# Performance work log

Hardware: AMD Instinct MI355X
Metric: run time of the kernel (lower is better)

The kernel has to match this reference:

```python
import jax, jax.numpy as jnp
import numpy as np

S = 1            # support_num
NEIGHBOR = 32    # neighbor_num for ball query
EPS = 1e-12

def _gather(t, idx):
    # t: (bs, N, C), idx: (bs, M, n) -> (bs, M, n, C)
    return jax.vmap(lambda tb, ib: tb[ib])(t, idx)

def _pick(t, idx):
    # t: (bs, M, C), idx: (bs, V) -> (bs, V, C)
    return jax.vmap(lambda tb, ib: tb[ib])(t, idx)

def _normalize(x, axis):
    return x / jnp.maximum(jnp.linalg.norm(x, axis=axis, keepdims=True), EPS)

def query_ball_point(radius, nsample, xyz, new_xyz):
    # PointNet++-style ball query: indices of first nsample points within radius,
    # missing slots filled with the first valid neighbor (self, since dist=0).
    sq = jnp.sum((new_xyz[:, :, None, :] - xyz[:, None, :, :]) ** 2, axis=-1)  # (bs,S,N)
    N = xyz.shape[1]
    idx = jnp.broadcast_to(jnp.arange(N), sq.shape)
    idx = jnp.where(sq > radius * radius, N, idx)
    idx = jnp.sort(idx, axis=-1)[:, :, :nsample]
    return jnp.where(idx == N, idx[:, :, :1], idx)

def _dir_norm(vertices, nbr_idx):
    nbrs = _gather(vertices, nbr_idx)                       # (bs,v,n,3)
    return _normalize(nbrs - vertices[:, :, None, :], axis=-1)

def conv_surface(nbr_idx, vertices, directions, K=32):
    # directions: (3, S*K)
    dn = _dir_norm(vertices, nbr_idx)
    theta = jax.nn.relu(jnp.einsum('bvnd,dk->bvnk', dn, _normalize(directions, 0)))
    bs, v, n, _ = theta.shape
    return theta.reshape(bs, v, n, S, K).max(axis=2).sum(axis=2)  # (bs,v,K)

def conv_layer(nbr_idx, vertices, fm, w, b, d, K=32):
    # w: (Cin,(S+1)*K), b: ((S+1)*K,), d: (3,S*K)
    dn = _dir_norm(vertices, nbr_idx)
    theta = jax.nn.relu(jnp.einsum('bvnd,dk->bvnk', dn, _normalize(d, 0)))  # (bs,v,n,S*K)
    f = jnp.einsum('bvc,ck->bvk', fm, w) + b                # (bs,v,(S+1)*K)
    center, support = f[..., :K], f[..., K:]
    sup = _gather(support, nbr_idx)                          # (bs,v,n,S*K)
    bs, v, n, _ = sup.shape
    act = (theta * sup).reshape(bs, v, n, S, K).max(axis=2).sum(axis=2)
    return center + act

def pool_layer(vertices, fm, radius, key, rate=4, nn_num=4):
    idx = query_ball_point(radius, nn_num, vertices, vertices)
    pooled = _gather(fm, idx).max(axis=2)                    # neighborhood max-pool
    v = vertices.shape[1]
    perm = jax.random.permutation(key, v)[: v // rate]       # random subsample (fixed key)
    return vertices[:, perm], pooled[:, perm]

def get_nearest_index(target, source):
    sq = jnp.sum((target[:, :, None, :] - source[:, None, :, :]) ** 2, axis=-1)
    return jnp.argmin(sq, axis=-1)                           # (bs, V_target)

def _forward(vertices, onehot, d0, w1, b1, dd1, w2, b2, dd2, w3, b3, dd3,
             w4, b4, dd4, w5, b5, dd5, w6, b6, dd6, w7, b7, dd7,
             cw1, cb1, cw2, cb2, cw3, cb3):
    relu = jax.nn.relu
    bs, V, _ = vertices.shape
    ni = query_ball_point(0.25, NEIGHBOR, vertices, vertices)
    fm0 = relu(conv_surface(ni, vertices, d0))
    fm1 = jnp.concatenate([fm0, relu(conv_layer(ni, vertices, fm0, w1, b1, dd1))], -1)
    fm2 = jnp.concatenate([fm1, relu(conv_layer(ni, vertices, fm1, w2, b2, dd2))], -1)
    v1, fp1 = pool_layer(vertices, fm2, 0.25, jax.random.fold_in(jax.random.key(42), 1))
    ni = query_ball_point(0.39, NEIGHBOR, v1, v1)
    fm3 = jnp.concatenate([fp1, relu(conv_layer(ni, v1, fp1, w3, b3, dd3))], -1)
    fm4 = jnp.concatenate([fm3, relu(conv_layer(ni, v1, fm3, w4, b4, dd4))], -1)
    fm5 = jnp.concatenate([fm4, relu(conv_layer(ni, v1, fm4, w5, b5, dd5))], -1)
    v2, fp2 = pool_layer(v1, fm5, 0.39, jax.random.fold_in(jax.random.key(42), 2))
    ni = query_ball_point(0.63, NEIGHBOR, v2, v2)
    fm6 = jnp.concatenate([fp2, relu(conv_layer(ni, v2, fp2, w6, b6, dd6))], -1)
    fm7 = jnp.concatenate([fm6, relu(conv_layer(ni, v2, fm6, w7, b7, dd7))], -1)
    f_global = fm7.max(axis=1)                               # (bs, 256)
    n1 = get_nearest_index(vertices, v1)
    n2 = get_nearest_index(vertices, v2)
    fuse = jnp.concatenate([
        fm0, fm1, fm2,
        _pick(fm3, n1), _pick(fm4, n1), _pick(fm5, n1),
        _pick(fm6, n2), _pick(fm7, n2),
        jnp.broadcast_to(f_global[:, None, :], (bs, V, f_global.shape[-1])),
        jnp.broadcast_to(onehot[:, None, :], (bs, V, onehot.shape[-1])),
    ], axis=-1)                                              # (bs, V, 1424)
    h = relu(jnp.einsum('bvc,oc->bvo', fuse, cw1) + cb1)
    h = relu(jnp.einsum('bvc,oc->bvo', h, cw2) + cb2)
    return jnp.einsum('bvc,oc->bvo', h, cw3) + cb3           # (bs, V, class_num)


def setup_inputs() -> dict:
    key = jax.random.key(0)
    ks = iter(jax.random.split(key, 40))
    bs, N, cat = 8, 2048, 16
    vertices = jax.random.uniform(next(ks), (bs, N, 3), dtype=jnp.float32)
    labels = jax.random.randint(next(ks), (bs,), 0, cat)
    onehot = jax.nn.one_hot(labels, cat, dtype=jnp.float32)
    def p(shape):
        return jax.random.normal(next(ks), shape, dtype=jnp.float32) * 0.05
    inp = {"vertices": vertices, "onehot": onehot, "d0": p((3, S * 32))}
    ins = [32, 64, 96, 128, 160, 192, 224]
    for i, c in enumerate(ins, start=1):
        inp[f"w{i}"] = p((c, (S + 1) * 32))
        inp[f"b{i}"] = p(((S + 1) * 32,))
        inp[f"dd{i}"] = p((3, S * 32))
    inp["cw1"] = p((1024, 1424)); inp["cb1"] = p((1024,))
    inp["cw2"] = p((512, 1024)); inp["cb2"] = p((512,))
    inp["cw3"] = p((50, 512)); inp["cb3"] = p((50,))
    return inp


def reference(vertices, onehot, d0, w1, b1, dd1, w2, b2, dd2, w3, b3, dd3,
              w4, b4, dd4, w5, b5, dd5, w6, b6, dd6, w7, b7, dd7,
              cw1, cb1, cw2, cb2, cw3, cb3):
    return _forward(vertices, onehot, d0, w1, b1, dd1, w2, b2, dd2, w3, b3, dd3,
                    w4, b4, dd4, w5, b5, dd5, w6, b6, dd6, w7, b7, dd7,
                    cw1, cb1, cw2, cb2, cw3, cb3)
```

## Files before the change

### kernel.cpp

```cpp
#include <hip/hip_runtime.h>
#include <hip/hip_bf16.h>

#define BS 8
#define V0 2048
#define V1N 512
#define V2N 128

typedef unsigned short ushort_t;
typedef __attribute__((ext_vector_type(8))) short bf16x8;
typedef __attribute__((ext_vector_type(4))) float f32x4;

__device__ __forceinline__ void tf2x32(unsigned k0, unsigned k1,
                                       unsigned x0, unsigned x1,
                                       unsigned &o0, unsigned &o1) {
  unsigned ks2 = k0 ^ k1 ^ 0x1BD11BDAu;
  x0 += k0; x1 += k1;
#define RR(r) { x0 += x1; x1 = (x1 << (r)) | (x1 >> (32 - (r))); x1 ^= x0; }
  RR(13) RR(15) RR(26) RR(6)   x0 += k1;  x1 += ks2 + 1u;
  RR(17) RR(29) RR(16) RR(24)  x0 += ks2; x1 += k0 + 2u;
  RR(13) RR(15) RR(26) RR(6)   x0 += k0;  x1 += k1 + 3u;
  RR(17) RR(29) RR(16) RR(24)  x0 += k1;  x1 += ks2 + 4u;
  RR(13) RR(15) RR(26) RR(6)   x0 += ks2; x1 += k0 + 5u;
#undef RR
  o0 = x0; o1 = x1;
}

__device__ __forceinline__ ushort_t f2bf(float f) {
  unsigned u = __float_as_uint(f);
  u += 0x7FFFu + ((u >> 16) & 1u);
  return (ushort_t)(u >> 16);
}

__device__ __forceinline__ float sqdist_f32(float cx, float cy, float cz,
                                            const float* p) {
  float dx = __fsub_rn(cx, p[0]);
  float dy = __fsub_rn(cy, p[1]);
  float dz = __fsub_rn(cz, p[2]);
  return __fadd_rn(__fadd_rn(__fmul_rn(dx, dx), __fmul_rn(dy, dy)),
                   __fmul_rn(dz, dz));
}

#define KP1 1472

#define PREP_BLKS 1025
#define QBP1_BLKS 512
__global__ __launch_bounds__(256) void misc1_kernel(
    int* __restrict__ rank, const float* __restrict__ cw1,
    const float* __restrict__ cw2, const float* __restrict__ cw3,
    const float* __restrict__ cb3, ushort_t* __restrict__ cw1b,
    ushort_t* __restrict__ cw2b, ushort_t* __restrict__ cw3b,
    float* __restrict__ cb3p, const float* __restrict__ pts,
    int* __restrict__ ni1) {
  int bid = blockIdx.x, tid = threadIdx.x;
  if (bid < 18) {
    __shared__ unsigned sb[2048];
    int seg, segfirst, n, base;
    if (bid < 8)       { seg = 0; segfirst = 0;  n = 2048; base = 0; }
    else if (bid < 16) { seg = 1; segfirst = 8;  n = 2048; base = 2048; }
    else               { seg = 2; segfirst = 16; n = 512;  base = 4096; }
    unsigned k0, k1, nk0, nk1, sk0, sk1;
    if (seg == 0) {
      tf2x32(0u, 42u, 0u, 1u, k0, k1);
      tf2x32(k0, k1, 0u, 1u, sk0, sk1);
    } else if (seg == 1) {
      tf2x32(0u, 42u, 0u, 1u, k0, k1);
      tf2x32(k0, k1, 0u, 0u, nk0, nk1);
      tf2x32(nk0, nk1, 0u, 1u, sk0, sk1);
    } else {
      tf2x32(0u, 42u, 0u, 2u, k0, k1);
      tf2x32(k0, k1, 0u, 1u, sk0, sk1);
    }
    for (int i = tid; i < n; i += 256) {
      unsigned o0, o1;
      tf2x32(sk0, sk1, 0u, (unsigned)i, o0, o1);
      sb[i] = o0 ^ o1;
    }
    __syncthreads();
    int tt = (bid - segfirst) * 256 + tid;
    unsigned bt = sb[tt];
    int cnt = 0;
#pragma unroll 8
    for (int s = 0; s < n; ++s) {
      unsigned bs = sb[s];
      cnt += (bs < bt) || (bs == bt && s < tt);
    }
    rank[base + tt] = cnt;
  } else if (bid < 18 + PREP_BLKS) {
    int c = (bid - 18) * 256 + tid;
    const int C1 = 1024 * (KP1 / 8);
    const int C2 = (512 * 1024) / 8;
    const int C3 = (128 * 512) / 8;
    if (c < C1) {
      int n = c / (KP1 / 8);
      int cc = c - n * (KP1 / 8);
      int k = cc * 8;
      bf16x8 o = (bf16x8){0, 0, 0, 0, 0, 0, 0, 0};
      if (k < 1424) {
        const float* src = cw1 + (size_t)n * 1424 + k;
        float4 lo = *(const float4*)src;
        float4 hi = *(const float4*)(src + 4);
        o[0] = (short)f2bf(lo.x); o[1] = (short)f2bf(lo.y);
        o[2] = (short)f2bf(lo.z); o[3] = (short)f2bf(lo.w);
        o[4] = (short)f2bf(hi.x); o[5] = (short)f2bf(hi.y);
        o[6] = (short)f2bf(hi.z); o[7] = (short)f2bf(hi.w);
      }
      *(bf16x8*)(cw1b + (size_t)c * 8) = o;
    } else if (c < C1 + C2) {
      int u = (c - C1) * 8;
      const float* src = cw2 + u;
      float4 lo = *(const float4*)src;
      float4 hi = *(const float4*)(src + 4);
      bf16x8 o;
      o[0] = (short)f2bf(lo.x); o[1] = (short)f2bf(lo.y);
      o[2] = (short)f2bf(lo.z); o[3] = (short)f2bf(lo.w);
      o[4] = (short)f2bf(hi.x); o[5] = (short)f2bf(hi.y);
      o[6] = (short)f2bf(hi.z); o[7] = (short)f2bf(hi.w);
      *(bf16x8*)(cw2b + u) = o;
    } else if (c < C1 + C2 + C3) {
      int u = (c - C1 - C2) * 8;
      int n = u >> 9, k = u & 511;
      bf16x8 o = (bf16x8){0, 0, 0, 0, 0, 0, 0, 0};
      if (n < 50) {
        const float* src = cw3 + (size_t)n * 512 + k;
        float4 lo = *(const float4*)src;
        float4 hi = *(const float4*)(src + 4);
        o[0] = (short)f2bf(lo.x); o[1] = (short)f2bf(lo.y);
        o[2] = (short)f2bf(lo.z); o[3] = (short)f2bf(lo.w);
        o[4] = (short)f2bf(hi.x); o[5] = (short)f2bf(hi.y);
        o[6] = (short)f2bf(hi.z); o[7] = (short)f2bf(hi.w);
      }
      *(bf16x8*)(cw3b + u) = o;
    } else if (c < C1 + C2 + C3 + 16) {
      int u = (c - C1 - C2 - C3) * 8;
#pragma unroll
      for (int e = 0; e < 8; ++e)
        cb3p[u + e] = (u + e) < 50 ? cb3[u + e] : 0.f;
    }
  } else {
    __shared__ float spts[V0 * 3];
    int bq = bid - 18 - PREP_BLKS;
    int qbase = bq * 32;
    int b = qbase >> 11;
    const float* base = pts + (size_t)b * V0 * 3;
    for (int i = tid; i < V0 * 3 / 4; i += 256)
      ((float4*)spts)[i] = ((const float4*)base)[i];
    __syncthreads();
    int lane = tid & 63, wv = tid >> 6;
    for (int rep = 0; rep < 8; ++rep) {
      int qoff = wv * 8 + rep;
      int qi = (qbase & 2047) + qoff;
      int wid = qbase + qoff;
      float cx = spts[qi * 3], cy = spts[qi * 3 + 1], cz = spts[qi * 3 + 2];
      int cnt = 0, idx0 = 0;
      for (int j0 = 0; j0 < V0; j0 += 64) {
        int j = j0 + lane;
        float d2 = sqdist_f32(cx, cy, cz, spts + (size_t)j * 3);
        bool in = (d2 <= 0.0625f);
        unsigned long long mask = __ballot(in);
        if (cnt == 0 && mask) idx0 = j0 + __builtin_ctzll(mask);
        if (in) {
          int rk = cnt + __popcll(mask & ((1ull << lane) - 1ull));
          if (rk < 32) ni1[(size_t)wid * 32 + rk] = j;
        }
        cnt += __popcll(mask);
        if (cnt >= 32) break;
      }
      for (int s = cnt + lane; s < 32; s += 64) ni1[(size_t)wid * 32 + s] = idx0;
    }
  }
}

__device__ __forceinline__ void dirn(const float* base, int v, int nb,
                                     float& ox, float& oy, float& oz) {
  float dx = __fsub_rn(base[nb * 3 + 0], base[v * 3 + 0]);
  float dy = __fsub_rn(base[nb * 3 + 1], base[v * 3 + 1]);
  float dz = __fsub_rn(base[nb * 3 + 2], base[v * 3 + 2]);
  float s2 = __fadd_rn(__fadd_rn(__fmul_rn(dx, dx), __fmul_rn(dy, dy)),
                       __fmul_rn(dz, dz));
  float nrm = fmaxf(__fsqrt_rn(s2), 1e-12f);
  ox = __fdiv_rn(dx, nrm); oy = __fdiv_rn(dy, nrm); oz = __fdiv_rn(dz, nrm);
}

__device__ __forceinline__ void norm_col(const float* d, int k,
                                         float& ox, float& oy, float& oz) {
  float x = d[k], y = d[32 + k], z = d[64 + k];
  float s2 = __fadd_rn(__fadd_rn(__fmul_rn(x, x), __fmul_rn(y, y)),
                       __fmul_rn(z, z));
  float nrm = fmaxf(__fsqrt_rn(s2), 1e-12f);
  ox = __fdiv_rn(x, nrm); oy = __fdiv_rn(y, nrm); oz = __fdiv_rn(z, nrm);
}

__global__ __launch_bounds__(256) void misc2_kernel(
    const int* __restrict__ rank, int* __restrict__ perm1,
    int* __restrict__ perm2, const float* __restrict__ pts,
    const int* __restrict__ ni, const float* __restrict__ d0,
    const float* __restrict__ w1, const float* __restrict__ b1,
    float* __restrict__ out, float* __restrict__ fn) {
  int bid = blockIdx.x, tid = threadIdx.x;
  if (bid == 0) {
    __shared__ int a1[2048];
    __shared__ int a2[2048];
    for (int i = tid; i < 2048; i += 256) a1[rank[i]] = i;
    __syncthreads();
    for (int i = tid; i < 2048; i += 256) a2[rank[2048 + i]] = a1[i];
    __syncthreads();
    for (int i = tid; i < 512; i += 256) perm1[i] = a2[i];
    for (int i = tid; i < 512; i += 256) a1[rank[4096 + i]] = i;
    __syncthreads();
    for (int i = tid; i < 128; i += 256) perm2[i] = a1[i];
    return;
  }
  __shared__ float sdir[3][32];
  __shared__ float sdn[8][32][3];
  __shared__ float sfm[8][32];
  if (tid < 32) {
    float x, y, z; norm_col(d0, tid, x, y, z);
    sdir[0][tid] = x; sdir[1][tid] = y; sdir[2][tid] = z;
  }
  int vloc = tid >> 5, k = tid & 31;
  size_t bvg = (size_t)(bid - 1) * 8 + vloc;
  int b = (int)(bvg >> 11), v = (int)(bvg & 2047);
  const float* base = pts + (size_t)b * V0 * 3;
  int nb = ni[bvg * 32 + k];
  float x, y, z; dirn(base, v, nb, x, y, z);
  sdn[vloc][k][0] = x; sdn[vloc][k][1] = y; sdn[vloc][k][2] = z;
  __syncthreads();
  float m = 0.f;
  for (int n = 0; n < 32; ++n) {
    float d = sdn[vloc][n][0] * sdir[0][k] + sdn[vloc][n][1] * sdir[1][k] +
              sdn[vloc][n][2] * sdir[2][k];
    m = fmaxf(m, fmaxf(d, 0.f));
  }
  out[bvg * 96 + k] = m;
  sfm[vloc][k] = m;
  __syncthreads();
  float a1v = b1[k], a2v = b1[k + 32];
  for (int c = 0; c < 32; ++c) {
    float vv = sfm[vloc][c];
    a1v += vv * w1[c * 64 + k];
    a2v += vv * w1[c * 64 + k + 32];
  }
  fn[bvg * 64 + k] = a1v;
  fn[bvg * 64 + k + 32] = a2v;
}

__global__ __launch_bounds__(256) void conv_act_kernel(
    const float* __restrict__ pts, const float* __restrict__ dd,
    const int* __restrict__ ni, const float* __restrict__ f,
    float* __restrict__ out, int Nv, int ldout, int colofs,
    const float* __restrict__ wn, const float* __restrict__ bn,
    float* __restrict__ fn) {
  __shared__ float sdir[3][32];
  __shared__ float sdn[8][32][3];
  __shared__ int sidx[8][32];
  __shared__ float sfm[8][256];
  int tid = threadIdx.x;
  if (tid < 32) {
    float x, y, z; norm_col(dd, tid, x, y, z);
    sdir[0][tid] = x; sdir[1][tid] = y; sdir[2][tid] = z;
  }
  int vloc = tid >> 5, k = tid & 31;
  size_t bvg = (size_t)blockIdx.x * 8 + vloc;
  int b = (int)(bvg / Nv), v = (int)(bvg % Nv);
  const float* base = pts + (size_t)b * Nv * 3;
  int nb = ni[bvg * 32 + k];
  float x, y, z; dirn(base, v, nb, x, y, z);
  sdn[vloc][k][0] = x; sdn[vloc][k][1] = y; sdn[vloc][k][2] = z;
  sidx[vloc][k] = nb;
  __syncthreads();
  float m = -INFINITY;
  size_t fb = (size_t)b * Nv * 64;
  for (int n = 0; n < 32; ++n) {
    float th = fmaxf(sdn[vloc][n][0] * sdir[0][k] + sdn[vloc][n][1] * sdir[1][k] +
                     sdn[vloc][n][2] * sdir[2][k], 0.f);
    float sup = f[fb + (size_t)sidx[vloc][n] * 64 + 32 + k];
    m = fmaxf(m, th * sup);
  }
  float center = f[bvg * 64 + k];
  float res = fmaxf(center + m, 0.f);
  out[bvg * ldout + colofs + k] = res;
  if (wn) {
    size_t rowbase = (size_t)blockIdx.x * 8;
#pragma unroll 1
    for (int r = 0; r < 8; ++r)
      if (tid < colofs) sfm[r][tid] = out[(rowbase + r) * ldout + tid];
    sfm[vloc][colofs + k] = res;
    __syncthreads();
    int cin = colofs + 32;
    float a1v = bn[k], a2v = bn[k + 32];
    for (int c = 0; c < cin; ++c) {
      float vv = sfm[vloc][c];
      a1v += vv * wn[c * 64 + k];
      a2v += vv * wn[c * 64 + k + 32];
    }
    fn[bvg * 64 + k] = a1v;
    fn[bvg * 64 + k + 32] = a2v;
  }
}

__global__ __launch_bounds__(256) void conv_act_qbp_kernel(
    const float* __restrict__ pts, int Nv, float rrq,
    const float* __restrict__ dd, int* __restrict__ ni_out,
    const float* __restrict__ f, float* __restrict__ out, int ldout,
    int colofs, const float* __restrict__ wn, const float* __restrict__ bn,
    float* __restrict__ fn) {
  __shared__ float spts[512 * 3];
  __shared__ float sdir[3][32];
  __shared__ float sdn[8][32][3];
  __shared__ int sni[8][32];
  __shared__ float sfm[8][256];
  int tid = threadIdx.x;
  int b = (blockIdx.x * 8) / Nv;
  int vbase = (blockIdx.x * 8) % Nv;
  const float* gp = pts + (size_t)b * Nv * 3;
  for (int i = tid; i < Nv * 3; i += 256) spts[i] = gp[i];
  if (tid < 32) {
    float x, y, z; norm_col(dd, tid, x, y, z);
    sdir[0][tid] = x; sdir[1][tid] = y; sdir[2][tid] = z;
  }
  __syncthreads();
  int lane = tid & 63, wv = tid >> 6;
  for (int rep = 0; rep < 2; ++rep) {
    int vl = wv * 2 + rep;
    int v = vbase + vl;
    float cx = spts[v * 3], cy = spts[v * 3 + 1], cz = spts[v * 3 + 2];
    int cnt = 0, idx0 = 0;
    for (int j0 = 0; j0 < Nv; j0 += 64) {
      int j = j0 + lane;
      float d2 = sqdist_f32(cx, cy, cz, spts + (size_t)j * 3);
      bool in = (d2 <= rrq);
      unsigned long long mask = __ballot(in);
      if (cnt == 0 && mask) idx0 = j0 + __builtin_ctzll(mask);
      if (in) {
        int rk = cnt + __popcll(mask & ((1ull << lane) - 1ull));
        if (rk < 32) sni[vl][rk] = j;
      }
      cnt += __popcll(mask);
      if (cnt >= 32) break;
    }
    for (int s = cnt + lane; s < 32; s += 64) sni[vl][s] = idx0;
  }
  __syncthreads();
  ni_out[(size_t)(blockIdx.x * 8) * 32 + tid] = sni[tid >> 5][tid & 31];
  int vloc = tid >> 5, k = tid & 31;
  size_t bvg = (size_t)blockIdx.x * 8 + vloc;
  int v = vbase + vloc;
  int nb = sni[vloc][k];
  float x, y, z; dirn(spts, v, nb, x, y, z);
  sdn[vloc][k][0] = x; sdn[vloc][k][1] = y; sdn[vloc][k][2] = z;
  __syncthreads();
  float m = -INFINITY;
  size_t fb = (size_t)b * Nv * 64;
  for (int n = 0; n < 32; ++n) {
    float th = fmaxf(sdn[vloc][n][0] * sdir[0][k] + sdn[vloc][n][1] * sdir[1][k] +
                     sdn[vloc][n][2] * sdir[2][k], 0.f);
    float sup = f[fb + (size_t)sni[vloc][n] * 64 + 32 + k];
    m = fmaxf(m, th * sup);
  }
  float center = f[bvg * 64 + k];
  float res = fmaxf(center + m, 0.f);
  out[bvg * ldout + colofs + k] = res;
  size_t rowbase = (size_t)blockIdx.x * 8;
#pragma unroll 1
  for (int r = 0; r < 8; ++r)
    if (tid < colofs) sfm[r][tid] = out[(rowbase + r) * ldout + tid];
  sfm[vloc][colofs + k] = res;
  __syncthreads();
  int cin = colofs + 32;
  float a1v = bn[k], a2v = bn[k + 32];
  for (int c = 0; c < cin; ++c) {
    float vv = sfm[vloc][c];
    a1v += vv * wn[c * 64 + k];
    a2v += vv * wn[c * 64 + k + 32];
  }
  fn[bvg * 64 + k] = a1v;
  fn[bvg * 64 + k + 32] = a2v;
}

__global__ __launch_bounds__(256) void pool_kernel(
    const float* __restrict__ pts_in, const float* __restrict__ fm_in,
    int ld_in, int C, int Nv_in, const int* __restrict__ perm, int Nv_out,
    float rr, float* __restrict__ pts_out, float* __restrict__ fm_out,
    int ld_out, const float* __restrict__ wn, const float* __restrict__ bn,
    float* __restrict__ fn) {
  __shared__ float spf[4][192];
  int wv = threadIdx.x >> 6;
  int lane = threadIdx.x & 63;
  int wid = blockIdx.x * 4 + wv;
  int b = wid / Nv_out, pp = wid - b * Nv_out;
  int v = perm[pp];
  const float* base = pts_in + (size_t)b * Nv_in * 3;
  float cx = base[v * 3], cy = base[v * 3 + 1], cz = base[v * 3 + 2];
  int nb[4]; int cnt = 0;
  for (int j0 = 0; j0 < Nv_in && cnt < 4; j0 += 64) {
    int j = j0 + lane;
    float d2 = sqdist_f32(cx, cy, cz, base + (size_t)j * 3);
    unsigned long long mask = __ballot(d2 <= rr);
    while (mask && cnt < 4) {
      int bp = __builtin_ctzll(mask);
      mask &= mask - 1;
      nb[cnt++] = j0 + bp;
    }
  }
  for (int q = cnt; q < 4; ++q) nb[q] = nb[0];
  if (lane < 3) pts_out[(size_t)wid * 3 + lane] = base[v * 3 + lane];
  size_t inrow = (size_t)b * Nv_in;
  size_t outrow = (size_t)wid * ld_out;
  for (int c = lane; c < C; c += 64) {
    float m = fm_in[(inrow + nb[0]) * ld_in + c];
    m = fmaxf(m, fm_in[(inrow + nb[1]) * ld_in + c]);
    m = fmaxf(m, fm_in[(inrow + nb[2]) * ld_in + c]);
    m = fmaxf(m, fm_in[(inrow + nb[3]) * ld_in + c]);
    fm_out[outrow + c] = m;
    spf[wv][c] = m;
  }
  __syncthreads();
  int o = threadIdx.x & 63, w_ = threadIdx.x >> 6;
  int wid0 = blockIdx.x * 4 + w_;
  float a = bn[o];
  for (int c = 0; c < C; ++c) a += spf[w_][c] * wn[c * 64 + o];
  fn[(size_t)wid0 * 64 + o] = a;
}

__global__ void gmax_kernel(const float* __restrict__ fm,
                            float* __restrict__ out) {
  int t = blockIdx.x * blockDim.x + threadIdx.x;
  if (t >= BS * 256) return;
  int b = t >> 8, c = t & 255;
  float m = -INFINITY;
  for (int v = 0; v < V2N; ++v)
    m = fmaxf(m, fm[((size_t)b * V2N + v) * 256 + c]);
  out[t] = m;
}

__global__ __launch_bounds__(256) void fuse_row_kernel(
    const float* __restrict__ fm2, const float* __restrict__ fm5,
    const float* __restrict__ fm7, const float* __restrict__ fglob,
    const float* __restrict__ onehot, const float* __restrict__ verts,
    const float* __restrict__ v1, const float* __restrict__ v2,
    ushort_t* __restrict__ fuse_b) {
  __shared__ unsigned long long red[256];
  __shared__ int sn1, sn2;
  int bv = blockIdx.x;
  int b = bv >> 11;
  int tid = threadIdx.x;
  float cx = verts[(size_t)bv * 3 + 0];
  float cy = verts[(size_t)bv * 3 + 1];
  float cz = verts[(size_t)bv * 3 + 2];
  unsigned long long best = ~0ull;
  const float* sb = v1 + (size_t)b * V1N * 3;
  for (int j = tid; j < V1N; j += 256) {
    float d2 = sqdist_f32(cx, cy, cz, sb + (size_t)j * 3);
    unsigned long long key =
        (((unsigned long long)__float_as_uint(d2)) << 32) | (unsigned)j;
    best = best < key ? best : key;
  }
  red[tid] = best;
  __syncthreads();
  for (int s = 128; s > 0; s >>= 1) {
    if (tid < s) red[tid] = red[tid] < red[tid + s] ? red[tid] : red[tid + s];
    __syncthreads();
  }
  if (tid == 0) sn1 = (int)(red[0] & 0xffffffffu);
  __syncthreads();
  best = ~0ull;
  sb = v2 + (size_t)b * V2N * 3;
  for (int j = tid; j < V2N; j += 256) {
    float d2 = sqdist_f32(cx, cy, cz, sb + (size_t)j * 3);
    unsigned long long key =
        (((unsigned long long)__float_as_uint(d2)) << 32) | (unsigned)j;
    best = best < key ? best : key;
  }
  red[tid] = best;
  __syncthreads();
  for (int s = 128; s > 0; s >>= 1) {
    if (tid < s) red[tid] = red[tid] < red[tid + s] ? red[tid] : red[tid + s];
    __syncthreads();
  }
  if (tid == 0) sn2 = (int)(red[0] & 0xffffffffu);
  __syncthreads();
  const float* r2 = fm2 + (size_t)bv * 96;
  const float* r5 = fm5 + ((size_t)b * V1N + sn1) * 192;
  const float* r7 = fm7 + ((size_t)b * V2N + sn2) * 256;
  const float* rg = fglob + b * 256;
  const float* roh = onehot + b * 16;
  if (tid < KP1 / 8) {
    int c = tid * 8;
    const float* src = nullptr;
    if (c < 192) {
      int cc = (c < 32) ? c : (c < 96 ? c - 32 : c - 96);
      src = r2 + cc;
    } else if (c < 672) {
      int cc = (c < 320) ? c - 192 : (c < 480 ? c - 320 : c - 480);
      src = r5 + cc;
    } else if (c < 1152) {
      int cc = (c < 896) ? c - 672 : c - 896;
      src = r7 + cc;
    } else if (c < 1408) {
      src = rg + (c - 1152);
    } else if (c < 1424) {
      src = roh + (c - 1408);
    }
    float4 lo = make_float4(0.f, 0.f, 0.f, 0.f), hi = lo;
    if (src) { lo = *(const float4*)src; hi = *(const float4*)(src + 4); }
    bf16x8 o;
    o[0] = (short)f2bf(lo.x); o[1] = (short)f2bf(lo.y);
    o[2] = (short)f2bf(lo.z); o[3] = (short)f2bf(lo.w);
    o[4] = (short)f2bf(hi.x); o[5] = (short)f2bf(hi.y);
    o[6] = (short)f2bf(hi.z); o[7] = (short)f2bf(hi.w);
    *(bf16x8*)(fuse_b + (size_t)bv * KP1 + c) = o;
  }
}

typedef const __attribute__((address_space(1))) unsigned int gas_u32;
typedef __attribute__((address_space(3))) unsigned int las_u32;

__global__ __launch_bounds__(256) void gemm_mfma_nt(
    const ushort_t* __restrict__ A, const ushort_t* __restrict__ B,
    const float* __restrict__ bias, ushort_t* __restrict__ Cb,
    float* __restrict__ Cf, int K, int ldc, int nvalid, int mode) {
  __shared__ ushort_t As[128 * 64];
  __shared__ ushort_t Bs[128 * 64];
  int tid = threadIdx.x;
  int lane = tid & 63, w = tid >> 6;
  int wm = (w >> 1) * 64, wn = (w & 1) * 64;
  int nb = gridDim.x;
  int flat = blockIdx.x + nb * blockIdx.y;
  int xcd = flat & 7, slot = flat >> 3;
  int nidx = slot % nb;
  int mband = xcd + 8 * (slot / nb);
  int bm = mband * 128, bn = nidx * 128;
  f32x4 acc[4][4];
#pragma unroll
  for (int i = 0; i < 4; ++i)
#pragma unroll
    for (int j = 0; j < 4; ++j) acc[i][j] = (f32x4){0.f, 0.f, 0.f, 0.f};

  const ushort_t* gA[4];
  const ushort_t* gB[4];
  ushort_t* lA[4];
  ushort_t* lB[4];
  int rsub = lane >> 3;
  int scol = ((lane & 7) ^ rsub) * 8;
#pragma unroll
  for (int g = 0; g < 4; ++g) {
    int r = w * 32 + g * 8 + rsub;
    gA[g] = A + (size_t)(bm + r) * K + scol;
    gB[g] = B + (size_t)(bn + r) * K + scol;
    lA[g] = As + (w * 32 + g * 8) * 64;
    lB[g] = Bs + (w * 32 + g * 8) * 64;
  }
  int rA = lane & 15, q = lane >> 4;
  int r7 = rA & 7;

  for (int k0 = 0; k0 < K; k0 += 64) {
#pragma unroll
    for (int g = 0; g < 4; ++g)
      __builtin_amdgcn_global_load_lds((gas_u32*)(gA[g] + k0), (las_u32*)lA[g],
                                       16, 0, 0);
#pragma unroll
    for (int g = 0; g < 4; ++g)
      __builtin_amdgcn_global_load_lds((gas_u32*)(gB[g] + k0), (las_u32*)lB[g],
                                       16, 0, 0);
    __syncthreads();
#pragma unroll
    for (int s = 0; s < 2; ++s) {
      int pc = ((s * 4 + q) ^ r7) * 8;
      bf16x8 af[4], bfr[4];
#pragma unroll
      for (int i = 0; i < 4; ++i)
        af[i] = *(const bf16x8*)(As + (wm + i * 16 + rA) * 64 + pc);
#pragma unroll
      for (int j = 0; j < 4; ++j)
        bfr[j] = *(const bf16x8*)(Bs + (wn + j * 16 + rA) * 64 + pc);
#pragma unroll
      for (int i = 0; i < 4; ++i)
#pragma unroll
        for (int j = 0; j < 4; ++j)
          acc[i][j] = __builtin_amdgcn_mfma_f32_16x16x32_bf16(af[i], bfr[j],
                                                              acc[i][j], 0, 0, 0);
    }
    __syncthreads();
  }

  int rowq = (lane >> 4) * 4;
  int coll = lane & 15;
#pragma unroll
  for (int i = 0; i < 4; ++i) {
#pragma unroll
    for (int j = 0; j < 4; ++j) {
      int col = bn + wn + j * 16 + coll;
      float bi = bias[col];
#pragma unroll
      for (int r = 0; r < 4; ++r) {
        int row = bm + wm + i * 16 + rowq + r;
        float v = acc[i][j][r] + bi;
        if (mode == 0) {
          Cb[(size_t)row * ldc + col] = f2bf(fmaxf(v, 0.f));
        } else if (col < nvalid) {
          Cf[(size_t)row * ldc + col] = v;
        }
      }
    }
  }
}

__global__ __launch_bounds__(512, 2) void gemm256_mfma_nt(
    const ushort_t* __restrict__ A, const ushort_t* __restrict__ B,
    const float* __restrict__ bias, ushort_t* __restrict__ Cb,
    int K, int ldc) {
  __shared__ ushort_t As[2 * 256 * 64];
  __shared__ ushort_t Bs[2 * 256 * 64];
  int tid = threadIdx.x;
  int lane = tid & 63, w = tid >> 6;
  int wm = (w >> 2) * 128, wn = (w & 3) * 64;

  int flat = blockIdx.x;
  int xcd = flat & 7, slot = flat >> 3;
  int nidx = slot & 3, mband = xcd + 8 * (slot >> 2);
  int bm = mband * 256, bn = nidx * 256;

  f32x4 acc[8][4];
#pragma unroll
  for (int i = 0; i < 8; ++i)
#pragma unroll
    for (int j = 0; j < 4; ++j) acc[i][j] = (f32x4){0.f, 0.f, 0.f, 0.f};

  int rloc = tid >> 3, cch = tid & 7;
  int gc = (cch ^ (rloc & 7)) * 8;
  const ushort_t* gA[4];
  const ushort_t* gB[4];
#pragma unroll
  for (int i = 0; i < 4; ++i) {
    gA[i] = A + (size_t)(bm + i * 64 + rloc) * K + gc;
    gB[i] = B + (size_t)(bn + i * 64 + rloc) * K + gc;
  }
  int lofs = tid * 8;

  int rA = lane & 15, r7 = lane & 7;
  int qlane = lane >> 4;
  int pc0 = (qlane ^ r7) * 8;
  int pc1 = ((4 + qlane) ^ r7) * 8;

  int NT = K >> 6;

#pragma unroll
  for (int i = 0; i < 4; ++i) {
    __builtin_amdgcn_global_load_lds((gas_u32*)gA[i],
                                     (las_u32*)(As + i * 4096 + lofs), 16, 0, 0);
    gA[i] += 64;
  }
#pragma unroll
  for (int i = 0; i < 4; ++i) {
    __builtin_amdgcn_global_load_lds((gas_u32*)gB[i],
                                     (las_u32*)(Bs + i * 4096 + lofs), 16, 0, 0);
    gB[i] += 64;
  }

  for (int t = 0; t < NT; ++t) {
    int doff = (t & 1) * 16384;
    int poff = doff ^ 16384;

    asm volatile("s_waitcnt vmcnt(0)" ::: "memory");
    __builtin_amdgcn_sched_barrier(0);
    __builtin_amdgcn_s_barrier();
    __builtin_amdgcn_sched_barrier(0);

    if (t + 1 < NT) {
#pragma unroll
      for (int i = 0; i < 4; ++i) {
        __builtin_amdgcn_global_load_lds(
            (gas_u32*)gA[i], (las_u32*)(As + poff + i * 4096 + lofs), 16, 0, 0);
        gA[i] += 64;
      }
#pragma unroll
      for (int i = 0; i < 4; ++i) {
        __builtin_amdgcn_global_load_lds(
            (gas_u32*)gB[i], (las_u32*)(Bs + poff + i * 4096 + lofs), 16, 0, 0);
        gB[i] += 64;
      }
    }

    const ushort_t* Ab = As + doff;
    const ushort_t* Bb = Bs + doff;
    bf16x8 bfr[2][4];
#pragma unroll
    for (int s = 0; s < 2; ++s) {
      int pcs = s ? pc1 : pc0;
#pragma unroll
      for (int fj = 0; fj < 4; ++fj)
        bfr[s][fj] = *(const bf16x8*)(Bb + (wn + fj * 16 + rA) * 64 + pcs);
    }
#pragma unroll
    for (int band = 0; band < 2; ++band) {
      bf16x8 afr[2][4];
#pragma unroll
      for (int s = 0; s < 2; ++s) {
        int pcs = s ? pc1 : pc0;
#pragma unroll
        for (int fi = 0; fi < 4; ++fi)
          afr[s][fi] = *(const bf16x8*)(Ab + (wm + band * 64 + fi * 16 + rA) * 64 + pcs);
      }
      __builtin_amdgcn_s_setprio(1);
#pragma unroll
      for (int s = 0; s < 2; ++s)
#pragma unroll
        for (int fi = 0; fi < 4; ++fi)
#pragma unroll
          for (int fj = 0; fj < 4; ++fj)
            acc[band * 4 + fi][fj] = __builtin_amdgcn_mfma_f32_16x16x32_bf16(
                afr[s][fi], bfr[s][fj], acc[band * 4 + fi][fj], 0, 0, 0);
      __builtin_amdgcn_s_setprio(0);
    }
    asm volatile("s_waitcnt lgkmcnt(0)" ::: "memory");
    __builtin_amdgcn_sched_barrier(0);
  }

  int rowq = (lane >> 4) * 4;
  int coll = lane & 15;
  float bi[4];
#pragma unroll
  for (int j = 0; j < 4; ++j) bi[j] = bias[bn + wn + j * 16 + coll];
#pragma unroll
  for (int i = 0; i < 8; ++i) {
#pragma unroll
    for (int j = 0; j < 4; ++j) {
      int col = bn + wn + j * 16 + coll;
#pragma unroll
      for (int r = 0; r < 4; ++r) {
        int row = bm + wm + i * 16 + rowq + r;
        float v = acc[i][j][r] + bi[j];
        Cb[(size_t)row * ldc + col] = f2bf(fmaxf(v, 0.f));
      }
    }
  }
}

extern "C" void kernel_launch(void* const* d_in, const int* in_sizes, int n_in,
                              void* d_out, int out_size, void* d_ws,
                              size_t ws_size, hipStream_t stream) {
  const float* vertices = (const float*)d_in[0];
  const float* onehot = (const float*)d_in[1];
  const float* d0 = (const float*)d_in[2];
  const float *w[8], *bb[8], *dd[8];
  for (int i = 1; i <= 7; ++i) {
    w[i] = (const float*)d_in[3 * i];
    bb[i] = (const float*)d_in[3 * i + 1];
    dd[i] = (const float*)d_in[3 * i + 2];
  }
  const float* cw1 = (const float*)d_in[24];
  const float* cb1 = (const float*)d_in[25];
  const float* cw2 = (const float*)d_in[26];
  const float* cb2 = (const float*)d_in[27];
  const float* cw3 = (const float*)d_in[28];
  const float* cb3 = (const float*)d_in[29];
  float* out = (float*)d_out;

  char* wsp = (char*)d_ws;
  size_t off = 0;
  auto alloc = [&](size_t bytes) -> void* {
    void* p = wsp + off;
    off += (bytes + 255) & ~(size_t)255;
    return p;
  };
  const int M = BS * V0;
  int* rank = (int*)alloc(4608 * 4);
  int* perm1 = (int*)alloc(512 * 4);
  int* perm2 = (int*)alloc(128 * 4);
  int* ni1 = (int*)alloc((size_t)BS * V0 * 32 * 4);
  int* ni2 = (int*)alloc((size_t)BS * V1N * 32 * 4);
  int* ni3 = (int*)alloc((size_t)BS * V2N * 32 * 4);
  float* fm2buf = (float*)alloc((size_t)BS * V0 * 96 * 4);
  float* fm5buf = (float*)alloc((size_t)BS * V1N * 192 * 4);
  float* fm7buf = (float*)alloc((size_t)BS * V2N * 256 * 4);
  float* fbuf = (float*)alloc((size_t)BS * V0 * 64 * 4);
  float* v1 = (float*)alloc((size_t)BS * V1N * 3 * 4);
  float* v2 = (float*)alloc((size_t)BS * V2N * 3 * 4);
  float* fglob = (float*)alloc((size_t)BS * 256 * 4);
  ushort_t* fuse_b = (ushort_t*)alloc((size_t)M * KP1 * 2);
  ushort_t* h1b = (ushort_t*)alloc((size_t)M * 1024 * 2);
  ushort_t* h2b = (ushort_t*)alloc((size_t)M * 512 * 2);
  ushort_t* cw1b = (ushort_t*)alloc((size_t)1024 * KP1 * 2);
  ushort_t* cw2b = (ushort_t*)alloc((size_t)512 * 1024 * 2);
  ushort_t* cw3b = (ushort_t*)alloc((size_t)128 * 512 * 2);
  float* cb3p = (float*)alloc(128 * 4);

  float rr1 = 0.0625f;
  float rr2 = (float)(0.39 * 0.39);
  float rr3 = (float)(0.63 * 0.63);

  misc1_kernel<<<18 + PREP_BLKS + QBP1_BLKS, 256, 0, stream>>>(
      rank, cw1, cw2, cw3, cb3, cw1b, cw2b, cw3b, cb3p, vertices, ni1);
  misc2_kernel<<<1 + BS * V0 / 8, 256, 0, stream>>>(
      rank, perm1, perm2, vertices, ni1, d0, w[1], bb[1], fm2buf, fbuf);
  conv_act_kernel<<<BS * V0 / 8, 256, 0, stream>>>(
      vertices, dd[1], ni1, fbuf, fm2buf, V0, 96, 32, w[2], bb[2], fbuf);
  conv_act_kernel<<<BS * V0 / 8, 256, 0, stream>>>(
      vertices, dd[2], ni1, fbuf, fm2buf, V0, 96, 64, nullptr, nullptr, nullptr);
  pool_kernel<<<BS * V1N / 4, 256, 0, stream>>>(
      vertices, fm2buf, 96, 96, V0, perm1, V1N, rr1, v1, fm5buf, 192,
      w[3], bb[3], fbuf);
  conv_act_qbp_kernel<<<BS * V1N / 8, 256, 0, stream>>>(
      v1, V1N, rr2, dd[3], ni2, fbuf, fm5buf, 192, 96, w[4], bb[4], fbuf);
  conv_act_kernel<<<BS * V1N / 8, 256, 0, stream>>>(
      v1, dd[4], ni2, fbuf, fm5buf, V1N, 192, 128, w[5], bb[5], fbuf);
  conv_act_kernel<<<BS * V1N / 8, 256, 0, stream>>>(
      v1, dd[5], ni2, fbuf, fm5buf, V1N, 192, 160, nullptr, nullptr, nullptr);
  pool_kernel<<<BS * V2N / 4, 256, 0, stream>>>(
      v1, fm5buf, 192, 192, V1N, perm2, V2N, rr2, v2, fm7buf, 256,
      w[6], bb[6], fbuf);
  conv_act_qbp_kernel<<<BS * V2N / 8, 256, 0, stream>>>(
      v2, V2N, rr3, dd[6], ni3, fbuf, fm7buf, 256, 192, w[7], bb[7], fbuf);
  conv_act_kernel<<<BS * V2N / 8, 256, 0, stream>>>(
      v2, dd[7], ni3, fbuf, fm7buf, V2N, 256, 224, nullptr, nullptr, nullptr);
  gmax_kernel<<<BS, 256, 0, stream>>>(fm7buf, fglob);
  fuse_row_kernel<<<M, 256, 0, stream>>>(fm2buf, fm5buf, fm7buf, fglob, onehot,
                                         vertices, v1, v2, fuse_b);
  gemm256_mfma_nt<<<(M / 256) * (1024 / 256), 512, 0, stream>>>(
      fuse_b, cw1b, cb1, h1b, KP1, 1024);
  gemm_mfma_nt<<<dim3(512 / 128, M / 128), 256, 0, stream>>>(
      h1b, cw2b, cb2, h2b, nullptr, 1024, 512, 512, 0);
  gemm_mfma_nt<<<dim3(1, M / 128), 256, 0, stream>>>(
      h2b, cw3b, cb3p, nullptr, out, 512, 50, 50, 1);
}
```

Before: 409.3 us.

## Replace 256-tile GEMM with 128-tile GEMM loading B directly from global

The first two MLP GEMMs now use a new 128x128-tile kernel that stages only A through LDS and reads B fragments straight from global memory (cached) into registers, with XCD-aware tile mapping. Smaller tiles and half the LDS per block are meant to raise occupancy and block count. The global max kernel is also split across 64 blocks with a shared-memory reduction instead of 8 serial blocks. The risk is that direct B loads go uncoalesced, and the smaller tiles give less reuse per block.

```diff
diff --git a/kernel.cpp b/kernel.cpp
--- a/kernel.cpp
+++ b/kernel.cpp
@@ -422,15 +422,22 @@
   fn[(size_t)wid0 * 64 + o] = a;
 }
 
-__global__ void gmax_kernel(const float* __restrict__ fm,
-                            float* __restrict__ out) {
-  int t = blockIdx.x * blockDim.x + threadIdx.x;
-  if (t >= BS * 256) return;
-  int b = t >> 8, c = t & 255;
+__global__ __launch_bounds__(256) void gmax_kernel(
+    const float* __restrict__ fm, float* __restrict__ out) {
+  __shared__ float red[8][32];
+  int b = blockIdx.x >> 3, cg = blockIdx.x & 7;
+  int vsub = threadIdx.x >> 5, cl = threadIdx.x & 31;
+  int c = cg * 32 + cl;
   float m = -INFINITY;
-  for (int v = 0; v < V2N; ++v)
+  for (int v = vsub; v < V2N; v += 8)
     m = fmaxf(m, fm[((size_t)b * V2N + v) * 256 + c]);
-  out[t] = m;
+  red[vsub][cl] = m;
+  __syncthreads();
+  if (vsub == 0) {
+#pragma unroll
+    for (int r = 1; r < 8; ++r) m = fmaxf(m, red[r][cl]);
+    out[b * 256 + c] = m;
+  }
 }
 
 __global__ __launch_bounds__(256) void fuse_row_kernel(
@@ -605,131 +612,109 @@
   }
 }
 
-__global__ __launch_bounds__(512, 2) void gemm256_mfma_nt(
+__global__ __launch_bounds__(256, 3) void gemm128_bdirect(
     const ushort_t* __restrict__ A, const ushort_t* __restrict__ B,
     const float* __restrict__ bias, ushort_t* __restrict__ Cb,
-    int K, int ldc) {
-  __shared__ ushort_t As[2 * 256 * 64];
-  __shared__ ushort_t Bs[2 * 256 * 64];
+    int K, int ldc, int nnt) {
+  __shared__ ushort_t As[2][128 * 64];
   int tid = threadIdx.x;
   int lane = tid & 63, w = tid >> 6;
-  int wm = (w >> 2) * 128, wn = (w & 3) * 64;
+  int wm = (w >> 1) * 64, wn = (w & 1) * 64;
 
   int flat = blockIdx.x;
   int xcd = flat & 7, slot = flat >> 3;
-  int nidx = slot & 3, mband = xcd + 8 * (slot >> 2);
-  int bm = mband * 256, bn = nidx * 256;
-
-  f32x4 acc[8][4];
-#pragma unroll
-  for (int i = 0; i < 8; ++i)
+  int nidx = slot % nnt, mband = xcd + 8 * (slot / nnt);
+  int bm = mband * 128, bn = nidx * 128;
+
+  f32x4 acc[4][4];
+#pragma unroll
+  for (int i = 0; i < 4; ++i)
 #pragma unroll
     for (int j = 0; j < 4; ++j) acc[i][j] = (f32x4){0.f, 0.f, 0.f, 0.f};
 
-  int rloc = tid >> 3, cch = tid & 7;
-  int gc = (cch ^ (rloc & 7)) * 8;
-  const ushort_t* gA[4];
-  const ushort_t* gB[4];
-#pragma unroll
-  for (int i = 0; i < 4; ++i) {
-    gA[i] = A + (size_t)(bm + i * 64 + rloc) * K + gc;
-    gB[i] = B + (size_t)(bn + i * 64 + rloc) * K + gc;
-  }
+  int rsub = tid >> 3, cch = tid & 7;
+  int gc = (cch ^ (rsub & 7)) * 8;
+  const ushort_t* gA = A + (size_t)(bm + rsub) * K + gc;
   int lofs = tid * 8;
 
-  int rA = lane & 15, r7 = lane & 7;
-  int qlane = lane >> 4;
+  int rA = lane & 15, qlane = lane >> 4, r7 = rA & 7;
   int pc0 = (qlane ^ r7) * 8;
   int pc1 = ((4 + qlane) ^ r7) * 8;
 
+  const ushort_t* Bw = B + (size_t)(bn + wn + rA) * K + qlane * 8;
+
   int NT = K >> 6;
 
 #pragma unroll
-  for (int i = 0; i < 4; ++i) {
-    __builtin_amdgcn_global_load_lds((gas_u32*)gA[i],
-                                     (las_u32*)(As + i * 4096 + lofs), 16, 0, 0);
-    gA[i] += 64;
-  }
-#pragma unroll
-  for (int i = 0; i < 4; ++i) {
-    __builtin_amdgcn_global_load_lds((gas_u32*)gB[i],
-                                     (las_u32*)(Bs + i * 4096 + lofs), 16, 0, 0);
-    gB[i] += 64;
-  }
+  for (int i = 0; i < 4; ++i)
+    __builtin_amdgcn_global_load_lds(
+        (gas_u32*)(gA + (size_t)i * 32 * K),
+        (las_u32*)(&As[0][i * 2048 + lofs]), 16, 0, 0);
 
   for (int t = 0; t < NT; ++t) {
-    int doff = (t & 1) * 16384;
-    int poff = doff ^ 16384;
+    int k0 = t * 64;
+    const ushort_t* Ab = &As[t & 1][0];
 
     asm volatile("s_waitcnt vmcnt(0)" ::: "memory");
     __builtin_amdgcn_sched_barrier(0);
     __builtin_amdgcn_s_barrier();
     __builtin_amdgcn_sched_barrier(0);
 
+    bf16x8 bfr0[4], bfr1[4];
+#pragma unroll
+    for (int fj = 0; fj < 4; ++fj)
+      bfr0[fj] = *(const bf16x8*)(Bw + (size_t)fj * 16 * K + k0);
+#pragma unroll
+    for (int fj = 0; fj < 4; ++fj)
+      bfr1[fj] = *(const bf16x8*)(Bw + (size_t)fj * 16 * K + k0 + 32);
+    __builtin_amdgcn_sched_barrier(0);
+
     if (t + 1 < NT) {
-#pragma unroll
-      for (int i = 0; i < 4; ++i) {
+      const ushort_t* gAn = gA + (size_t)(t + 1) * 64;
+      ushort_t* dst = &As[(t + 1) & 1][0];
+#pragma unroll
+      for (int i = 0; i < 4; ++i)
         __builtin_amdgcn_global_load_lds(
-            (gas_u32*)gA[i], (las_u32*)(As + poff + i * 4096 + lofs), 16, 0, 0);
-        gA[i] += 64;
-      }
-#pragma unroll
-      for (int i = 0; i < 4; ++i) {
-        __builtin_amdgcn_global_load_lds(
-            (gas_u32*)gB[i], (las_u32*)(Bs + poff + i * 4096 + lofs), 16, 0, 0);
-        gB[i] += 64;
-      }
-    }
-
-    const ushort_t* Ab = As + doff;
-    const ushort_t* Bb = Bs + doff;
-    bf16x8 bfr[2][4];
-#pragma unroll
-    for (int s = 0; s < 2; ++s) {
-      int pcs = s ? pc1 : pc0;
+            (gas_u32*)(gAn + (size_t)i * 32 * K),
+            (las_u32*)(dst + i * 2048 + lofs), 16, 0, 0);
+    }
+
+    bf16x8 a[4];
+#pragma unroll
+    for (int fi = 0; fi < 4; ++fi)
+      a[fi] = *(const bf16x8*)(Ab + (wm + fi * 16 + rA) * 64 + pc0);
+#pragma unroll
+    for (int fi = 0; fi < 4; ++fi)
 #pragma unroll
       for (int fj = 0; fj < 4; ++fj)
-        bfr[s][fj] = *(const bf16x8*)(Bb + (wn + fj * 16 + rA) * 64 + pcs);
-    }
-#pragma unroll
-    for (int band = 0; band < 2; ++band) {
-      bf16x8 afr[2][4];
-#pragma unroll
-      for (int s = 0; s < 2; ++s) {
-        int pcs = s ? pc1 : pc0;
-#pragma unroll
-        for (int fi = 0; fi < 4; ++fi)
-          afr[s][fi] = *(const bf16x8*)(Ab + (wm + band * 64 + fi * 16 + rA) * 64 + pcs);
-      }
-      __builtin_amdgcn_s_setprio(1);
-#pragma unroll
-      for (int s = 0; s < 2; ++s)
-#pragma unroll
-        for (int fi = 0; fi < 4; ++fi)
-#pragma unroll
-          for (int fj = 0; fj < 4; ++fj)
-            acc[band * 4 + fi][fj] = __builtin_amdgcn_mfma_f32_16x16x32_bf16(
-                afr[s][fi], bfr[s][fj], acc[band * 4 + fi][fj], 0, 0, 0);
-      __builtin_amdgcn_s_setprio(0);
-    }
+        acc[fi][fj] = __builtin_amdgcn_mfma_f32_16x16x32_bf16(
+            a[fi], bfr0[fj], acc[fi][fj], 0, 0, 0);
+#pragma unroll
+    for (int fi = 0; fi < 4; ++fi)
+      a[fi] = *(const bf16x8*)(Ab + (wm + fi * 16 + rA) * 64 + pc1);
+#pragma unroll
+    for (int fi = 0; fi < 4; ++fi)
+#pragma unroll
+      for (int fj = 0; fj < 4; ++fj)
+        acc[fi][fj] = __builtin_amdgcn_mfma_f32_16x16x32_bf16(
+            a[fi], bfr1[fj], acc[fi][fj], 0, 0, 0);
+
     asm volatile("s_waitcnt lgkmcnt(0)" ::: "memory");
     __builtin_amdgcn_sched_barrier(0);
   }
 
   int rowq = (lane >> 4) * 4;
   int coll = lane & 15;
-  float bi[4];
-#pragma unroll
-  for (int j = 0; j < 4; ++j) bi[j] = bias[bn + wn + j * 16 + coll];
-#pragma unroll
-  for (int i = 0; i < 8; ++i) {
+#pragma unroll
+  for (int i = 0; i < 4; ++i) {
 #pragma unroll
     for (int j = 0; j < 4; ++j) {
       int col = bn + wn + j * 16 + coll;
+      float bi = bias[col];
 #pragma unroll
       for (int r = 0; r < 4; ++r) {
         int row = bm + wm + i * 16 + rowq + r;
-        float v = acc[i][j][r] + bi[j];
+        float v = acc[i][j][r] + bi;
         Cb[(size_t)row * ldc + col] = f2bf(fmaxf(v, 0.f));
       }
     }
@@ -813,13 +798,13 @@
       v2, V2N, rr3, dd[6], ni3, fbuf, fm7buf, 256, 192, w[7], bb[7], fbuf);
   conv_act_kernel<<<BS * V2N / 8, 256, 0, stream>>>(
       v2, dd[7], ni3, fbuf, fm7buf, V2N, 256, 224, nullptr, nullptr, nullptr);
-  gmax_kernel<<<BS, 256, 0, stream>>>(fm7buf, fglob);
+  gmax_kernel<<<64, 256, 0, stream>>>(fm7buf, fglob);
   fuse_row_kernel<<<M, 256, 0, stream>>>(fm2buf, fm5buf, fm7buf, fglob, onehot,
                                          vertices, v1, v2, fuse_b);
-  gemm256_mfma_nt<<<(M / 256) * (1024 / 256), 512, 0, stream>>>(
-      fuse_b, cw1b, cb1, h1b, KP1, 1024);
-  gemm_mfma_nt<<<dim3(512 / 128, M / 128), 256, 0, stream>>>(
-      h1b, cw2b, cb2, h2b, nullptr, 1024, 512, 512, 0);
+  gemm128_bdirect<<<(M / 128) * (1024 / 128), 256, 0, stream>>>(
+      fuse_b, cw1b, cb1, h1b, KP1, 1024, 1024 / 128);
+  gemm128_bdirect<<<(M / 128) * (512 / 128), 256, 0, stream>>>(
+      h1b, cw2b, cb2, h2b, 1024, 512, 512 / 128);
   gemm_mfma_nt<<<dim3(1, M / 128), 256, 0, stream>>>(
       h2b, cw3b, cb3p, nullptr, out, 512, 50, 50, 1);
 }
```

After: 459.4 us. +12.3%, slower.
